# Performance work log

Measured on AMD Instinct MI355X. Metric: run time of the kernel, lower is better.

## Reference

```python
import jax, jax.numpy as jnp
import numpy as np

KS = 3          # kernel_size
DIL = 1         # dilation
PAD = DIL * (KS - 1) // 2
HEAD_DIM = 64
SCALE = HEAD_DIM ** (-0.5)


def _unfold_patches(x):
    """Emulate nn.Unfold(KS, DIL, PAD, 1): x [B,d,H,W] -> [B,d,KS*KS,H,W] (zero-padded)."""
    B, d, H, W = x.shape
    xp = jnp.pad(x, ((0, 0), (0, 0), (PAD, PAD), (PAD, PAD)))
    # small fixed loop over the KS*KS kernel offsets (9 slices), same patch order as Unfold
    patches = [xp[:, :, i * DIL:i * DIL + H, j * DIL:j * DIL + W]
               for i in range(KS) for j in range(KS)]
    return jnp.stack(patches, axis=2)  # [B, d, KS*KS, H, W]


def setup_inputs() -> dict:
    key = jax.random.key(0)
    kq, kk, kv = jax.random.split(key, 3)
    shape = (32, 64, 64, 64)  # [B, head_dim, H, W]
    return {
        "q": jax.random.normal(kq, shape, dtype=jnp.float32),
        "k": jax.random.normal(kk, shape, dtype=jnp.float32),
        "v": jax.random.normal(kv, shape, dtype=jnp.float32),
    }


def reference(q, k, v):
    # q: [B,d,H,W]; per-pixel attention over the KS*KS dilated neighborhood of k/v
    k_p = _unfold_patches(k)                                   # [B,d,n,H,W], n = KS*KS
    attn = jnp.einsum('bdhw,bdnhw->bnhw', q, k_p) * SCALE      # [B,n,H,W]
    attn = jax.nn.softmax(attn, axis=1)                        # softmax over window (dim=-1 in torch layout)
    v_p = _unfold_patches(v)                                   # [B,d,n,H,W]
    out = jnp.einsum('bnhw,bdnhw->bdhw', attn, v_p)            # [B,d,H,W]
    return out
```

## Files before the change

### kernel.cpp

```cpp
#include <hip/hip_runtime.h>

namespace {
constexpr int Bn = 32, Dn = 64, Hn = 64, Wn = 64;
constexpr int PLANE = Hn * Wn;
constexpr int NW  = 4;
constexpr int DPW = Dn / NW;
constexpr float SCALE = 0.125f;
}

__global__ __launch_bounds__(256, 8) void dilate_attn_kernel(
    const float* __restrict__ q, const float* __restrict__ k,
    const float* __restrict__ v, float* __restrict__ out)
{
    __shared__ float red[9][NW][Wn];

    const int t  = threadIdx.x;
    const int w  = t & 63;
    const int wv = t >> 6;

    const int bid = blockIdx.x;
    const int swz = (bid & 7) * ((Bn * Hn) >> 3) + (bid >> 3);
    const int b = swz >> 6;
    const int h = swz & 63;

    const int base = b * Dn * PLANE;
    const int pix  = h * Wn + w;

    const bool up_ok = (h > 0), dn_ok = (h < Hn - 1);
    const bool lf_ok = (w > 0), rt_ok = (w < Wn - 1);

    float attn[9];
#pragma unroll
    for (int n = 0; n < 9; ++n) attn[n] = 0.0f;

    {
        const float* qd = q + base + (wv * DPW) * PLANE + pix;
        const float* kd = k + base + (wv * DPW) * PLANE + pix;
#pragma unroll 4
        for (int ds = 0; ds < DPW; ++ds) {
            const float qv = qd[ds * PLANE];
            const float* kc = kd + ds * PLANE;
#pragma unroll
            for (int di = 0; di < 3; ++di) {
                const bool okh = (di == 0) ? up_ok : (di == 2) ? dn_ok : true;
                const int  ro  = (di - 1) * Wn;
#pragma unroll
                for (int dj = 0; dj < 3; ++dj) {
                    const bool okw = (dj == 0) ? lf_ok : (dj == 2) ? rt_ok : true;
                    const float kv = (okh && okw) ? kc[ro + dj - 1] : 0.0f;
                    attn[di * 3 + dj] = fmaf(qv, kv, attn[di * 3 + dj]);
                }
            }
        }
    }

#pragma unroll
    for (int n = 0; n < 9; ++n) red[n][wv][w] = attn[n];
    __syncthreads();
#pragma unroll
    for (int n = 0; n < 9; ++n)
        attn[n] = (red[n][0][w] + red[n][1][w]) + (red[n][2][w] + red[n][3][w]);

#pragma unroll
    for (int n = 0; n < 9; ++n) attn[n] *= SCALE;
    float m = attn[0];
#pragma unroll
    for (int n = 1; n < 9; ++n) m = fmaxf(m, attn[n]);
    float s = 0.0f;
#pragma unroll
    for (int n = 0; n < 9; ++n) { attn[n] = __expf(attn[n] - m); s += attn[n]; }
    const float inv = 1.0f / s;
#pragma unroll
    for (int n = 0; n < 9; ++n) attn[n] *= inv;

    {
        const float* vd = v + base + (wv * DPW) * PLANE + pix;
        float* od = out + base + (wv * DPW) * PLANE + pix;
#pragma unroll 4
        for (int ds = 0; ds < DPW; ++ds) {
            const float* vc = vd + ds * PLANE;
            float acc = 0.0f;
#pragma unroll
            for (int di = 0; di < 3; ++di) {
                const bool okh = (di == 0) ? up_ok : (di == 2) ? dn_ok : true;
                const int  ro  = (di - 1) * Wn;
#pragma unroll
                for (int dj = 0; dj < 3; ++dj) {
                    const bool okw = (dj == 0) ? lf_ok : (dj == 2) ? rt_ok : true;
                    const float vv = (okh && okw) ? vc[ro + dj - 1] : 0.0f;
                    acc = fmaf(attn[di * 3 + dj], vv, acc);
                }
            }
            od[ds * PLANE] = acc;
        }
    }
}

extern "C" void kernel_launch(void* const* d_in, const int* in_sizes, int n_in,
                              void* d_out, int out_size, void* d_ws, size_t ws_size,
                              hipStream_t stream) {
    const float* q = (const float*)d_in[0];
    const float* k = (const float*)d_in[1];
    const float* v = (const float*)d_in[2];
    float* out = (float*)d_out;
    (void)in_sizes; (void)n_in; (void)out_size; (void)d_ws; (void)ws_size;

    const int grid = Bn * Hn;
    dilate_attn_kernel<<<grid, 256, 0, stream>>>(q, k, v, out);
}
```

Baseline: 31.53 us.

## Compute two pixels per thread with vectorized 4-wide neighborhood loads

Each thread now handles two adjacent output columns, and each block covers two rows. A thread loads one 4-float vector per kernel row, replacing nine scalar loads, and reuses those values across both pixels. Border handling moves from predicated loads to clamped addresses, with masking applied to the logits before the softmax and to the weights after it. The launch grid is halved and the occupancy hint lowered to 4 blocks. This cuts load instruction count and redundant neighbor loads, but raises register pressure and adds unaligned vector loads.

```diff
diff --git a/kernel.cpp b/kernel.cpp
--- a/kernel.cpp
+++ b/kernel.cpp
@@ -6,92 +6,147 @@
 constexpr int NW  = 4;
 constexpr int DPW = Dn / NW;
 constexpr float SCALE = 0.125f;
+typedef float f4a __attribute__((ext_vector_type(4), aligned(4)));
 }
 
-__global__ __launch_bounds__(256, 8) void dilate_attn_kernel(
+__global__ __launch_bounds__(256, 4) void dilate_attn_kernel(
     const float* __restrict__ q, const float* __restrict__ k,
     const float* __restrict__ v, float* __restrict__ out)
 {
-    __shared__ float red[9][NW][Wn];
+    __shared__ float2 red[NW][9][64];
 
     const int t  = threadIdx.x;
-    const int w  = t & 63;
+    const int l  = t & 63;
     const int wv = t >> 6;
+    const int ci = l & 31;
+    const int lr = l >> 5;
+    const int c  = ci * 2;
 
     const int bid = blockIdx.x;
-    const int swz = (bid & 7) * ((Bn * Hn) >> 3) + (bid >> 3);
-    const int b = swz >> 6;
-    const int h = swz & 63;
+    const int swz = (bid & 7) * 128 + (bid >> 3);
+    const int b      = swz >> 5;
+    const int stripe = swz & 31;
+    const int hr     = stripe * 2 + lr;
 
-    const int base = b * Dn * PLANE;
-    const int pix  = h * Wn + w;
+    const int  base = b * Dn * PLANE;
+    const bool ci0 = (ci == 0), ci31 = (ci == 31);
 
-    const bool up_ok = (h > 0), dn_ok = (h < Hn - 1);
-    const bool lf_ok = (w > 0), rt_ok = (w < Wn - 1);
+    const int cb = ci0 ? 0 : (ci31 ? (c - 2) : (c - 1));
 
-    float attn[9];
+    int  koff[3];
+    bool rok[3];
 #pragma unroll
-    for (int n = 0; n < 9; ++n) attn[n] = 0.0f;
+    for (int di = 0; di < 3; ++di) {
+        const int kr = hr - 1 + di;
+        rok[di] = (kr >= 0) && (kr < Hn);
+        const int krc = min(max(kr, 0), Hn - 1);
+        koff[di] = krc * Wn + cb;
+    }
+    const int qoff = hr * Wn + c;
+
+    float a0[9], a1[9];
+#pragma unroll
+    for (int n = 0; n < 9; ++n) { a0[n] = 0.0f; a1[n] = 0.0f; }
 
     {
-        const float* qd = q + base + (wv * DPW) * PLANE + pix;
-        const float* kd = k + base + (wv * DPW) * PLANE + pix;
+        const float* kp = k + base + wv * DPW * PLANE;
+        const float* qp = q + base + wv * DPW * PLANE;
 #pragma unroll 4
         for (int ds = 0; ds < DPW; ++ds) {
-            const float qv = qd[ds * PLANE];
-            const float* kc = kd + ds * PLANE;
+            const f4a r0 = *(const f4a*)(kp + koff[0]);
+            const f4a r1 = *(const f4a*)(kp + koff[1]);
+            const f4a r2 = *(const f4a*)(kp + koff[2]);
+            const float2 qv = *(const float2*)(qp + qoff);
+            kp += PLANE; qp += PLANE;
 #pragma unroll
             for (int di = 0; di < 3; ++di) {
-                const bool okh = (di == 0) ? up_ok : (di == 2) ? dn_ok : true;
-                const int  ro  = (di - 1) * Wn;
-#pragma unroll
-                for (int dj = 0; dj < 3; ++dj) {
-                    const bool okw = (dj == 0) ? lf_ok : (dj == 2) ? rt_ok : true;
-                    const float kv = (okh && okw) ? kc[ro + dj - 1] : 0.0f;
-                    attn[di * 3 + dj] = fmaf(qv, kv, attn[di * 3 + dj]);
-                }
+                const f4a vv = (di == 0) ? r0 : (di == 1) ? r1 : r2;
+                const float w0 = ci31 ? vv.y : vv.x;
+                const float w1 = ci0 ? vv.x : (ci31 ? vv.z : vv.y);
+                const float w2 = ci0 ? vv.y : (ci31 ? vv.w : vv.z);
+                const float w3 = ci0 ? vv.z : vv.w;
+                a0[di * 3 + 0] = fmaf(qv.x, w0, a0[di * 3 + 0]);
+                a0[di * 3 + 1] = fmaf(qv.x, w1, a0[di * 3 + 1]);
+                a0[di * 3 + 2] = fmaf(qv.x, w2, a0[di * 3 + 2]);
+                a1[di * 3 + 0] = fmaf(qv.y, w1, a1[di * 3 + 0]);
+                a1[di * 3 + 1] = fmaf(qv.y, w2, a1[di * 3 + 1]);
+                a1[di * 3 + 2] = fmaf(qv.y, w3, a1[di * 3 + 2]);
             }
         }
     }
 
 #pragma unroll
-    for (int n = 0; n < 9; ++n) red[n][wv][w] = attn[n];
+    for (int n = 0; n < 9; ++n) red[wv][n][l] = make_float2(a0[n], a1[n]);
     __syncthreads();
 #pragma unroll
-    for (int n = 0; n < 9; ++n)
-        attn[n] = (red[n][0][w] + red[n][1][w]) + (red[n][2][w] + red[n][3][w]);
+    for (int n = 0; n < 9; ++n) {
+        float2 s = red[0][n][l];
+#pragma unroll
+        for (int ow = 1; ow < NW; ++ow) {
+            const float2 p = red[ow][n][l];
+            s.x += p.x; s.y += p.y;
+        }
+        a0[n] = s.x; a1[n] = s.y;
+    }
 
 #pragma unroll
-    for (int n = 0; n < 9; ++n) attn[n] *= SCALE;
-    float m = attn[0];
+    for (int di = 0; di < 3; ++di)
 #pragma unroll
-    for (int n = 1; n < 9; ++n) m = fmaxf(m, attn[n]);
-    float s = 0.0f;
+        for (int dj = 0; dj < 3; ++dj) {
+            const int n = di * 3 + dj;
+            a0[n] = (rok[di] && (dj != 0 || !ci0))  ? a0[n] : 0.0f;
+            a1[n] = (rok[di] && (dj != 2 || !ci31)) ? a1[n] : 0.0f;
+        }
 #pragma unroll
-    for (int n = 0; n < 9; ++n) { attn[n] = __expf(attn[n] - m); s += attn[n]; }
-    const float inv = 1.0f / s;
+    for (int n = 0; n < 9; ++n) { a0[n] *= SCALE; a1[n] *= SCALE; }
+    float m0 = a0[0], m1 = a1[0];
 #pragma unroll
-    for (int n = 0; n < 9; ++n) attn[n] *= inv;
+    for (int n = 1; n < 9; ++n) { m0 = fmaxf(m0, a0[n]); m1 = fmaxf(m1, a1[n]); }
+    float s0 = 0.0f, s1 = 0.0f;
+#pragma unroll
+    for (int n = 0; n < 9; ++n) {
+        a0[n] = __expf(a0[n] - m0); s0 += a0[n];
+        a1[n] = __expf(a1[n] - m1); s1 += a1[n];
+    }
+    const float i0 = 1.0f / s0, i1 = 1.0f / s1;
+#pragma unroll
+    for (int n = 0; n < 9; ++n) { a0[n] *= i0; a1[n] *= i1; }
+
+#pragma unroll
+    for (int di = 0; di < 3; ++di)
+#pragma unroll
+        for (int dj = 0; dj < 3; ++dj) {
+            const int n = di * 3 + dj;
+            a0[n] = (rok[di] && (dj != 0 || !ci0))  ? a0[n] : 0.0f;
+            a1[n] = (rok[di] && (dj != 2 || !ci31)) ? a1[n] : 0.0f;
+        }
 
     {
-        const float* vd = v + base + (wv * DPW) * PLANE + pix;
-        float* od = out + base + (wv * DPW) * PLANE + pix;
+        const float* vp = v + base + wv * DPW * PLANE;
+        float*       op = out + base + wv * DPW * PLANE;
 #pragma unroll 4
         for (int ds = 0; ds < DPW; ++ds) {
-            const float* vc = vd + ds * PLANE;
-            float acc = 0.0f;
+            const f4a r0 = *(const f4a*)(vp + koff[0]);
+            const f4a r1 = *(const f4a*)(vp + koff[1]);
+            const f4a r2 = *(const f4a*)(vp + koff[2]);
+            vp += PLANE;
+            float o0 = 0.0f, o1 = 0.0f;
 #pragma unroll
             for (int di = 0; di < 3; ++di) {
-                const bool okh = (di == 0) ? up_ok : (di == 2) ? dn_ok : true;
-                const int  ro  = (di - 1) * Wn;
-#pragma unroll
-                for (int dj = 0; dj < 3; ++dj) {
-                    const bool okw = (dj == 0) ? lf_ok : (dj == 2) ? rt_ok : true;
-                    const float vv = (okh && okw) ? vc[ro + dj - 1] : 0.0f;
-                    acc = fmaf(attn[di * 3 + dj], vv, acc);
-                }
+                const f4a vv = (di == 0) ? r0 : (di == 1) ? r1 : r2;
+                const float w0 = ci31 ? vv.y : vv.x;
+                const float w1 = ci0 ? vv.x : (ci31 ? vv.z : vv.y);
+                const float w2 = ci0 ? vv.y : (ci31 ? vv.w : vv.z);
+                const float w3 = ci0 ? vv.z : vv.w;
+                o0 = fmaf(a0[di * 3 + 0], w0, o0);
+                o0 = fmaf(a0[di * 3 + 1], w1, o0);
+                o0 = fmaf(a0[di * 3 + 2], w2, o0);
+                o1 = fmaf(a1[di * 3 + 0], w1, o1);
+                o1 = fmaf(a1[di * 3 + 1], w2, o1);
+                o1 = fmaf(a1[di * 3 + 2], w3, o1);
             }
-            od[ds * PLANE] = acc;
+            *(float2*)(op + qoff) = make_float2(o0, o1);
+            op += PLANE;
         }
     }
 }
@@ -105,6 +160,6 @@
     float* out = (float*)d_out;
     (void)in_sizes; (void)n_in; (void)out_size; (void)d_ws; (void)ws_size;
 
-    const int grid = Bn * Hn;
+    const int grid = Bn * 32;
     dilate_attn_kernel<<<grid, 256, 0, stream>>>(q, k, v, out);
 }
```

New measurement: 30.14 us. -4.4%, faster.
